# Kernel optimization log

Hardware: AMD Instinct MI355X
Metric: run time of the kernel (lower is better)

The kernel has to match this reference:

```python
import jax, jax.numpy as jnp
import numpy as np
from jax import lax

EPS = 1e-8  # numerical safety in squash sqrt (torch repo uses plain sqrt)

def squash(s, axis=-1):
    sq = jnp.sum(s * s, axis=axis, keepdims=True)
    return (sq / (1.0 + sq)) * s / jnp.sqrt(sq + EPS)

def conv2d(x, w, b, stride):
    y = lax.conv_general_dilated(x, w, (stride, stride), 'VALID',
                                 dimension_numbers=('NCHW', 'OIHW', 'NCHW'))
    return y + b[None, :, None, None]

def setup_inputs() -> dict:
    key = jax.random.key(0)
    ks = jax.random.split(key, 12)
    B = 256
    x = jax.random.normal(ks[0], (B, 1, 28, 28), dtype=jnp.float32)
    conv_w = jax.random.normal(ks[1], (256, 1, 9, 9), dtype=jnp.float32) * 0.05
    conv_b = jnp.zeros((256,), dtype=jnp.float32)
    caps1_w = jax.random.normal(ks[2], (32, 8, 256, 9, 9), dtype=jnp.float32) * 0.01
    caps1_b = jnp.zeros((32, 8), dtype=jnp.float32)
    caps2_w = jax.random.normal(ks[3], (10, 1152, 8, 16), dtype=jnp.float32)  # torch.randn
    dec_w1 = jax.random.normal(ks[4], (160, 512), dtype=jnp.float32) * 0.05
    dec_b1 = jnp.zeros((512,), dtype=jnp.float32)
    dec_w2 = jax.random.normal(ks[5], (512, 1024), dtype=jnp.float32) * 0.04
    dec_b2 = jnp.zeros((1024,), dtype=jnp.float32)
    dec_w3 = jax.random.normal(ks[6], (1024, 784), dtype=jnp.float32) * 0.03
    dec_b3 = jnp.zeros((784,), dtype=jnp.float32)
    return {"x": x, "conv_w": conv_w, "conv_b": conv_b, "caps1_w": caps1_w,
            "caps1_b": caps1_b, "caps2_w": caps2_w, "dec_w1": dec_w1,
            "dec_b1": dec_b1, "dec_w2": dec_w2, "dec_b2": dec_b2,
            "dec_w3": dec_w3, "dec_b3": dec_b3}

def reference(x, conv_w, conv_b, caps1_w, caps1_b, caps2_w,
              dec_w1, dec_b1, dec_w2, dec_b2, dec_w3, dec_b3):
    B = x.shape[0]
    # conv + relu -> [B,256,20,20]
    h = jax.nn.relu(conv2d(x, conv_w, conv_b, 1))
    # CapsLayerOne: 32 parallel convs folded into one grouped-out conv -> [B,256,6,6]
    u = conv2d(h, caps1_w.reshape(32 * 8, 256, 9, 9), caps1_b.reshape(-1), 2)
    u = u.reshape(B, 32, 8, 6, 6)                    # [B,caps,ch,h,w]
    # replicate torch cat(dim=-1).view(B,8,-1): flatten order (h, caps, w) per channel
    u = u.transpose(0, 2, 3, 1, 4).reshape(B, 8, 1152)  # [B,8,N]
    u = squash(u.transpose(0, 2, 1))                 # [B,N,8], N=1152
    # CapsLayerTwo dynamic routing
    x_hat = jnp.einsum('bni,cnio->cbno', u, caps2_w)[:, :, :, None, :]  # [10,B,N,1,16]
    b = jnp.zeros_like(x_hat)
    v = None
    for i in range(3):
        c = jax.nn.softmax(b, axis=2)
        s = jnp.sum(x_hat * c, axis=2, keepdims=True)  # [10,B,1,1,16]
        v = squash(s)
        if i != 2:
            b = b + jnp.sum(x_hat * v, axis=-1, keepdims=True)
    v = v[:, :, 0, 0, :].transpose(1, 0, 2)            # [B,10,16]
    class_scores = jnp.sqrt(jnp.sum(v * v, axis=-1) + EPS)  # [B,10]
    class_probabilities = jax.nn.softmax(class_scores, axis=-1)
    labels = jnp.argmax(class_probabilities, axis=1)
    y = jax.nn.one_hot(labels, 10, dtype=v.dtype)
    masked = (v * y[:, :, None]).reshape(B, 160)
    d = jax.nn.relu(masked @ dec_w1 + dec_b1)
    d = jax.nn.relu(d @ dec_w2 + dec_b2)
    reconstructions = jax.nn.sigmoid(d @ dec_w3 + dec_b3)  # [B,784]
    return (class_probabilities, reconstructions)
```

## Files before the change

kernel.cpp:

```cpp
#include <hip/hip_runtime.h>
#include <cstdint>
#include <cstddef>

#define EPSF 1e-8f

typedef __attribute__((ext_vector_type(8))) short bf16x8;
typedef __attribute__((ext_vector_type(4))) float f32x4;
typedef unsigned short ushort_t;

static __device__ __forceinline__ ushort_t f2bf(float f) {
  unsigned u = __builtin_bit_cast(unsigned, f);
  unsigned r = (u + 0x7FFFu + ((u >> 16) & 1u)) >> 16;
  return (ushort_t)r;
}
static __device__ __forceinline__ float bf2f(ushort_t h) {
  return __builtin_bit_cast(float, (unsigned)h << 16);
}

__global__ __launch_bounds__(256) void conv1_kernel(
    const float* __restrict__ x, const float* __restrict__ cw,
    const float* __restrict__ cb, ushort_t* __restrict__ h2hi, ushort_t* __restrict__ h2lo)
{
  int oy = blockIdx.x, b = blockIdx.y, ci = threadIdx.x;
  float w[81];
#pragma unroll
  for (int i = 0; i < 81; ++i) w[i] = cw[ci * 81 + i];
  float bias = cb[ci];
  float acc[20];
#pragma unroll
  for (int ox = 0; ox < 20; ++ox) acc[ox] = bias;
  const float* xb = x + (size_t)b * 784;
  for (int ky = 0; ky < 9; ++ky) {
    const float* row = xb + (oy + ky) * 28;
    float rv[28];
#pragma unroll
    for (int c = 0; c < 28; ++c) rv[c] = row[c];
#pragma unroll
    for (int kx = 0; kx < 9; ++kx) {
      float wv = w[ky * 9 + kx];
#pragma unroll
      for (int ox = 0; ox < 20; ++ox)
        acc[ox] = fmaf(rv[ox + kx], wv, acc[ox]);
    }
  }
#pragma unroll
  for (int ox = 0; ox < 20; ++ox) {
    float a = fmaxf(acc[ox], 0.f);
    ushort_t hi = f2bf(a);
    ushort_t lo = f2bf(a - bf2f(hi));
    size_t o = ((size_t)(b * 400 + oy * 20 + ox)) * 256 + ci;
    h2hi[o] = hi; h2lo[o] = lo;
  }
}

__global__ __launch_bounds__(256) void w2k_prep_kernel(
    const float* __restrict__ c1w, ushort_t* __restrict__ w2khi, ushort_t* __restrict__ w2klo)
{
  int co = blockIdx.x, ci = threadIdx.x;
  const float* src = c1w + ((size_t)co * 256 + ci) * 81;
  size_t dst = (size_t)co * 20736 + ci;
  for (int tap = 0; tap < 81; ++tap) {
    float v = src[tap];
    ushort_t hi = f2bf(v);
    w2khi[dst + (size_t)tap * 256] = hi;
    w2klo[dst + (size_t)tap * 256] = f2bf(v - bf2f(hi));
  }
}

__global__ __launch_bounds__(512, 1) void caps1_mfma_kernel(
    const ushort_t* __restrict__ h2hi, const ushort_t* __restrict__ h2lo,
    const ushort_t* __restrict__ w2khi, const ushort_t* __restrict__ w2klo,
    float* __restrict__ partial)
{
  int bid = blockIdx.x;
  int ks8  = bid & 7;
  int ks   = ks8 >> 1;
  int ktap = ks8 & 1;
  int rest = bid >> 3;
  int mt = rest & 1;
  int nt = (rest >> 1) & 1;
  int pos = rest >> 2;
  int ys = pos / 6, xs = pos % 6;
  int t = threadIdx.x;
  int wid = t >> 6, lane = t & 63;
  int wrow = wid >> 2, wcol = wid & 3;
  int lrow = lane & 15, g = lane >> 4;

  int b0 = mt * 128, n0 = nt * 128, cib = ks * 64;
  int tb    = ktap ? 41 : 0;
  int ntaps = ktap ? 40 : 41;

  __shared__ ushort_t lds[2][4][128 * 64];

  f32x4 acc[4][2];
#pragma unroll
  for (int i = 0; i < 4; ++i)
#pragma unroll
    for (int j = 0; j < 2; ++j) acc[i][j] = (f32x4){0.f, 0.f, 0.f, 0.f};

  int c_ = (t & 7) ^ ((t >> 3) & 7);
  size_t aRow[2], bRow[2];
  int ldsBase[2];
#pragma unroll
  for (int i = 0; i < 2; ++i) {
    int row = i * 64 + (t >> 3);
    aRow[i] = (size_t)(b0 + row) * 400 * 256 + cib + c_ * 8;
    bRow[i] = (size_t)(n0 + row) * 20736 + cib + c_ * 8;
    ldsBase[i] = (i * 64 + wid * 8) * 64;
  }

  auto stage = [&](int tap, int bufi) {
    int ky = tap / 9, kx = tap - ky * 9;
    int pix = (2 * ys + ky) * 20 + 2 * xs + kx;
    size_t aoff = (size_t)pix * 256;
    size_t boff = (size_t)tap * 256;
#pragma unroll
    for (int i = 0; i < 2; ++i) {
      __builtin_amdgcn_global_load_lds(h2hi + aRow[i] + aoff, &lds[bufi][0][ldsBase[i]], 16, 0, 0);
      __builtin_amdgcn_global_load_lds(h2lo + aRow[i] + aoff, &lds[bufi][1][ldsBase[i]], 16, 0, 0);
      __builtin_amdgcn_global_load_lds(w2khi + bRow[i] + boff, &lds[bufi][2][ldsBase[i]], 16, 0, 0);
      __builtin_amdgcn_global_load_lds(w2klo + bRow[i] + boff, &lds[bufi][3][ldsBase[i]], 16, 0, 0);
    }
  };

  stage(tb + 0, 0);
  stage(tb + 1, 1);
  asm volatile("s_waitcnt vmcnt(8)" ::: "memory");
  __builtin_amdgcn_sched_barrier(0);
  __builtin_amdgcn_s_barrier();

  for (int j = 0; j < ntaps; ++j) {
    int cur = j & 1;
    const ushort_t* LAh = &lds[cur][0][0];
    const ushort_t* LAl = &lds[cur][1][0];
    const ushort_t* LBh = &lds[cur][2][0];
    const ushort_t* LBl = &lds[cur][3][0];
    bf16x8 a_h[2][4], a_l[2][4], b_h[2][2], b_l[2][2];
#pragma unroll
    for (int kseg = 0; kseg < 2; ++kseg) {
#pragma unroll
      for (int mf = 0; mf < 4; ++mf) {
        int off = (wrow * 64 + mf * 16 + lrow) * 64 + ((kseg * 4 + g) ^ (lrow & 7)) * 8;
        a_h[kseg][mf] = *(const bf16x8*)(LAh + off);
        a_l[kseg][mf] = *(const bf16x8*)(LAl + off);
      }
#pragma unroll
      for (int nf = 0; nf < 2; ++nf) {
        int off = (wcol * 32 + nf * 16 + lrow) * 64 + ((kseg * 4 + g) ^ (lrow & 7)) * 8;
        b_h[kseg][nf] = *(const bf16x8*)(LBh + off);
        b_l[kseg][nf] = *(const bf16x8*)(LBl + off);
      }
    }
    asm volatile("s_waitcnt lgkmcnt(0)" ::: "memory");
    __builtin_amdgcn_sched_barrier(0);
    __builtin_amdgcn_s_barrier();

    if (j + 2 < ntaps) stage(tb + j + 2, cur);
    __builtin_amdgcn_sched_barrier(0);

    __builtin_amdgcn_s_setprio(1);
#pragma unroll
    for (int kseg = 0; kseg < 2; ++kseg)
#pragma unroll
      for (int mf = 0; mf < 4; ++mf)
#pragma unroll
        for (int nf = 0; nf < 2; ++nf) {
          acc[mf][nf] = __builtin_amdgcn_mfma_f32_16x16x32_bf16(a_h[kseg][mf], b_h[kseg][nf], acc[mf][nf], 0, 0, 0);
          acc[mf][nf] = __builtin_amdgcn_mfma_f32_16x16x32_bf16(a_h[kseg][mf], b_l[kseg][nf], acc[mf][nf], 0, 0, 0);
          acc[mf][nf] = __builtin_amdgcn_mfma_f32_16x16x32_bf16(a_l[kseg][mf], b_h[kseg][nf], acc[mf][nf], 0, 0, 0);
        }
    __builtin_amdgcn_s_setprio(0);
    __builtin_amdgcn_sched_barrier(0);

    if (j + 2 < ntaps) { asm volatile("s_waitcnt vmcnt(8)" ::: "memory"); }
    else               { asm volatile("s_waitcnt vmcnt(0)" ::: "memory"); }
    __builtin_amdgcn_sched_barrier(0);
    __builtin_amdgcn_s_barrier();
  }

  float* pp = partial + (size_t)ks8 * 2359296;
#pragma unroll
  for (int mf = 0; mf < 4; ++mf) {
    int m = b0 + wrow * 64 + mf * 16 + g * 4;
#pragma unroll
    for (int nf = 0; nf < 2; ++nf) {
      int n = n0 + wcol * 32 + nf * 16 + lrow;
#pragma unroll
      for (int r = 0; r < 4; ++r)
        pp[((size_t)(pos * 256 + m + r)) * 256 + n] = acc[mf][nf][r];
    }
  }
}

__global__ __launch_bounds__(256) void combine_kernel(
    const float* __restrict__ partial, const float* __restrict__ c1b, float* __restrict__ u)
{
  int gidx = blockIdx.x * 256 + threadIdx.x;
  int caps = gidx & 31;
  int b = (gidx >> 5) & 255;
  int pos = gidx >> 13;
  int ys = pos / 6, xs = pos % 6;
  size_t base = ((size_t)pos * 256 + b) * 256 + caps * 8;
  f32x4 s0 = {0.f, 0.f, 0.f, 0.f}, s1 = {0.f, 0.f, 0.f, 0.f};
#pragma unroll
  for (int ksp = 0; ksp < 8; ++ksp) {
    const float* pp = partial + (size_t)ksp * 2359296 + base;
    s0 += *(const f32x4*)pp;
    s1 += *(const f32x4*)(pp + 4);
  }
  const float* bp = c1b + caps * 8;
#pragma unroll
  for (int i = 0; i < 4; ++i) { s0[i] += bp[i]; s1[i] += bp[4 + i]; }
  float sq = s0[0]*s0[0] + s0[1]*s0[1] + s0[2]*s0[2] + s0[3]*s0[3]
           + s1[0]*s1[0] + s1[1]*s1[1] + s1[2]*s1[2] + s1[3]*s1[3];
  float scale = sq / ((1.f + sq) * sqrtf(sq + EPSF));
  int nvec = ys * 192 + caps * 6 + xs;
  float* up = u + ((size_t)b * 1152 + nvec) * 8;
  f32x4 o0, o1;
#pragma unroll
  for (int i = 0; i < 4; ++i) { o0[i] = s0[i] * scale; o1[i] = s1[i] * scale; }
  *(f32x4*)up = o0;
  *(f32x4*)(up + 4) = o1;
}

__global__ __launch_bounds__(320) void xhat_kernel(
    const float* __restrict__ u, const float* __restrict__ W2, float* __restrict__ xh)
{
  int np = blockIdx.x;
  int t = threadIdx.x;
  int nh = t / 160;
  int r  = t % 160;
  int c = r >> 4, o = r & 15;
  int n = np * 2 + nh;
  __shared__ float us[2][256][8];
  for (int e = t; e < 4096; e += 320) {
    int b = e >> 4;
    int nn = (e >> 3) & 1, i = e & 7;
    us[nn][b][i] = u[((size_t)b * 1152 + np * 2 + nn) * 8 + i];
  }
  __syncthreads();
  float wcol[8];
  const float* wp = W2 + (((size_t)c * 1152 + n) * 8) * 16 + o;
#pragma unroll
  for (int i = 0; i < 8; ++i) wcol[i] = wp[i * 16];
  float* xp = xh + ((size_t)(c * 256) * 1152 + n) * 16 + o;
  for (int b = 0; b < 256; ++b) {
    float s = 0.f;
#pragma unroll
    for (int i = 0; i < 8; ++i) s = fmaf(us[nh][b][i], wcol[i], s);
    xp[(size_t)b * 1152 * 16] = s;
  }
}

__global__ __launch_bounds__(256) void routing_kernel(
    const float* __restrict__ xhat, float* __restrict__ vout)
{
  int b = blockIdx.x, c = blockIdx.y, t = threadIdx.x;
  int wid = t >> 6, lane = t & 63;
  float xh[5][16];
  float bn[5] = {0, 0, 0, 0, 0};
  bool valid[5];
  const float* xp = xhat + ((size_t)(c * 256 + b)) * 1152 * 16;
#pragma unroll
  for (int j = 0; j < 5; ++j) {
    int n = t + 256 * j;
    valid[j] = (n < 1152);
    if (valid[j]) {
      const f32x4* q = (const f32x4*)(xp + (size_t)n * 16);
#pragma unroll
      for (int v4 = 0; v4 < 4; ++v4) {
        f32x4 val = q[v4];
#pragma unroll
        for (int k = 0; k < 4; ++k) xh[j][v4 * 4 + k] = val[k];
      }
    } else {
#pragma unroll
      for (int o = 0; o < 16; ++o) xh[j][o] = 0.f;
    }
  }
  __shared__ float redm[4], redz[4], reds[64], sv[16];
  float scale = 0.f;
  for (int it = 0; it < 3; ++it) {
    float m = -1e30f;
#pragma unroll
    for (int j = 0; j < 5; ++j) if (valid[j]) m = fmaxf(m, bn[j]);
    for (int d = 1; d < 64; d <<= 1) m = fmaxf(m, __shfl_xor(m, d));
    if (lane == 0) redm[wid] = m;
    __syncthreads();
    m = fmaxf(fmaxf(redm[0], redm[1]), fmaxf(redm[2], redm[3]));
    float e[5]; float z = 0.f;
#pragma unroll
    for (int j = 0; j < 5; ++j) { e[j] = valid[j] ? expf(bn[j] - m) : 0.f; z += e[j]; }
    for (int d = 1; d < 64; d <<= 1) z += __shfl_xor(z, d);
    if (lane == 0) redz[wid] = z;
    __syncthreads();
    z = redz[0] + redz[1] + redz[2] + redz[3];
    float ps[16];
#pragma unroll
    for (int o = 0; o < 16; ++o) ps[o] = 0.f;
#pragma unroll
    for (int j = 0; j < 5; ++j)
#pragma unroll
      for (int o = 0; o < 16; ++o) ps[o] = fmaf(e[j], xh[j][o], ps[o]);
#pragma unroll
    for (int o = 0; o < 16; ++o) {
      float vv = ps[o];
      for (int d = 1; d < 64; d <<= 1) vv += __shfl_xor(vv, d);
      if (lane == 0) reds[wid * 16 + o] = vv;
    }
    __syncthreads();
    if (t < 16) sv[t] = (reds[t] + reds[16 + t] + reds[32 + t] + reds[48 + t]) / z;
    __syncthreads();
    float vsc[16]; float sq = 0.f;
#pragma unroll
    for (int o = 0; o < 16; ++o) { vsc[o] = sv[o]; sq += sv[o] * sv[o]; }
    scale = sq / ((1.f + sq) * sqrtf(sq + EPSF));
    if (it < 2) {
#pragma unroll
      for (int j = 0; j < 5; ++j) if (valid[j]) {
        float dot = 0.f;
#pragma unroll
        for (int o = 0; o < 16; ++o) dot = fmaf(xh[j][o], vsc[o] * scale, dot);
        bn[j] += dot;
      }
    }
    __syncthreads();
  }
  if (t < 16) vout[((size_t)c * 256 + b) * 16 + t] = sv[t] * scale;
}

__global__ __launch_bounds__(256) void classify_kernel(
    const float* __restrict__ v, float* __restrict__ probs, float* __restrict__ masked)
{
  int b = blockIdx.x, t = threadIdx.x;
  __shared__ float sc[10], vv[160];
  int c = t >> 4, o = t & 15;
  float val = 0.f;
  if (t < 160) { val = v[((size_t)c * 256 + b) * 16 + o]; vv[t] = val; }
  float sq = val * val;
  sq += __shfl_xor(sq, 1); sq += __shfl_xor(sq, 2);
  sq += __shfl_xor(sq, 4); sq += __shfl_xor(sq, 8);
  if (t < 160 && o == 0) sc[c] = sqrtf(sq + EPSF);
  __syncthreads();
  float m = sc[0];
#pragma unroll
  for (int i = 1; i < 10; ++i) m = fmaxf(m, sc[i]);
  float ee[10]; float Z = 0.f;
#pragma unroll
  for (int i = 0; i < 10; ++i) { ee[i] = expf(sc[i] - m); Z += ee[i]; }
  float p[10];
#pragma unroll
  for (int i = 0; i < 10; ++i) p[i] = ee[i] / Z;
  int label = 0; float best = p[0];
#pragma unroll
  for (int i = 1; i < 10; ++i) if (p[i] > best) { best = p[i]; label = i; }
  if (t < 10) probs[(size_t)b * 10 + t] = p[t];
  if (t < 160) masked[(size_t)b * 160 + t] = (c == label) ? vv[t] : 0.f;
}

template <int ACT>
__global__ __launch_bounds__(256) void mlp_kernel(
    const float* __restrict__ A, const float* __restrict__ W,
    const float* __restrict__ bias, float* __restrict__ C, int N, int K)
{
  int j = blockIdx.x * 64 + (threadIdx.x & 63);
  int ty = threadIdx.x >> 6;
  int m0 = blockIdx.y * 16;
  __shared__ float As[16][33];
  float acc[4] = {0.f, 0.f, 0.f, 0.f};
  for (int k0 = 0; k0 < K; k0 += 32) {
    for (int e = threadIdx.x; e < 512; e += 256) {
      int r = e >> 5, kk = e & 31;
      As[r][kk] = A[(size_t)(m0 + r) * K + k0 + kk];
    }
    __syncthreads();
    if (j < N) {
      for (int kk = 0; kk < 32; ++kk) {
        float wv = W[(size_t)(k0 + kk) * N + j];
#pragma unroll
        for (int r = 0; r < 4; ++r) acc[r] = fmaf(As[ty + 4 * r][kk], wv, acc[r]);
      }
    }
    __syncthreads();
  }
  if (j < N) {
    float bv = bias[j];
#pragma unroll
    for (int r = 0; r < 4; ++r) {
      float xx = acc[r] + bv;
      if (ACT == 0) xx = fmaxf(xx, 0.f);
      else xx = 1.f / (1.f + expf(-xx));
      C[(size_t)(m0 + ty + 4 * r) * N + j] = xx;
    }
  }
}

extern "C" void kernel_launch(void* const* d_in, const int* in_sizes, int n_in,
                              void* d_out, int out_size, void* d_ws, size_t ws_size,
                              hipStream_t stream)
{
  const float* x   = (const float*)d_in[0];
  const float* cw  = (const float*)d_in[1];
  const float* cb  = (const float*)d_in[2];
  const float* c1w = (const float*)d_in[3];
  const float* c1b = (const float*)d_in[4];
  const float* c2w = (const float*)d_in[5];
  const float* w1  = (const float*)d_in[6];
  const float* b1  = (const float*)d_in[7];
  const float* w2  = (const float*)d_in[8];
  const float* b2  = (const float*)d_in[9];
  const float* w3  = (const float*)d_in[10];
  const float* b3  = (const float*)d_in[11];
  float* out = (float*)d_out;

  char* p = (char*)d_ws;
  float* xh = (float*)p;
  ushort_t* h2hi  = (ushort_t*)p; p += (size_t)26214400 * 2;
  ushort_t* h2lo  = (ushort_t*)p; p += (size_t)26214400 * 2;
  ushort_t* w2khi = (ushort_t*)p; p += (size_t)5308416 * 2;
  ushort_t* w2klo = (ushort_t*)p; p += (size_t)5308416 * 2;
  float* partial  = (float*)p;    p += (size_t)8 * 2359296 * 4;
  float* u        = (float*)p;    p += (size_t)2359296 * 4;
  float* v        = (float*)p;    p += (size_t)40960 * 4;
  float* masked   = (float*)p;    p += (size_t)40960 * 4;
  float* a1       = (float*)p;    p += (size_t)131072 * 4;
  float* a2       = (float*)p;    p += (size_t)262144 * 4;

  hipLaunchKernelGGL(w2k_prep_kernel, dim3(256), dim3(256), 0, stream, c1w, w2khi, w2klo);
  hipLaunchKernelGGL(conv1_kernel, dim3(20, 256), dim3(256), 0, stream, x, cw, cb, h2hi, h2lo);
  hipLaunchKernelGGL(caps1_mfma_kernel, dim3(1152), dim3(512), 0, stream, h2hi, h2lo, w2khi, w2klo, partial);
  hipLaunchKernelGGL(combine_kernel, dim3(1152), dim3(256), 0, stream, partial, c1b, u);
  hipLaunchKernelGGL(xhat_kernel, dim3(576), dim3(320), 0, stream, u, c2w, xh);
  hipLaunchKernelGGL(routing_kernel, dim3(256, 10), dim3(256), 0, stream, xh, v);
  hipLaunchKernelGGL(classify_kernel, dim3(256), dim3(256), 0, stream, v, out, masked);
  hipLaunchKernelGGL(mlp_kernel<0>, dim3(8, 16), dim3(256), 0, stream, masked, w1, b1, a1, 512, 160);
  hipLaunchKernelGGL(mlp_kernel<0>, dim3(16, 16), dim3(256), 0, stream, a1, w2, b2, a2, 1024, 512);
  hipLaunchKernelGGL(mlp_kernel<1>, dim3(13, 16), dim3(256), 0, stream, a2, w3, b3, out + 2560, 784, 1024);
}
```

Before: 623.5 us.

## Use 4 waves with 64x64 warp tiles and overlap LDS fragment reads with MFMA

The caps1 MFMA kernel drops from 8 to 4 waves per block, and each wave now computes a 64x64 tile with a 4x4 accumulator array. Each thread therefore issues twice as many global-to-LDS loads. The main loop is restructured so the next tile's global stage is issued first. Fragments for the next buffer are then read from LDS between the two k-segment MFMA batches, so LDS reads overlap with MFMA work. This raises register pressure and halves the waves available to hide latency, in exchange for more MFMA work per LDS read and software-pipelined fragment loads.

```diff
diff --git a/kernel.cpp b/kernel.cpp
--- a/kernel.cpp
+++ b/kernel.cpp
@@ -67,7 +67,7 @@
   }
 }
 
-__global__ __launch_bounds__(512, 1) void caps1_mfma_kernel(
+__global__ __launch_bounds__(256, 1) void caps1_mfma_kernel(
     const ushort_t* __restrict__ h2hi, const ushort_t* __restrict__ h2lo,
     const ushort_t* __restrict__ w2khi, const ushort_t* __restrict__ w2klo,
     float* __restrict__ partial)
@@ -83,7 +83,7 @@
   int ys = pos / 6, xs = pos % 6;
   int t = threadIdx.x;
   int wid = t >> 6, lane = t & 63;
-  int wrow = wid >> 2, wcol = wid & 3;
+  int wr = wid >> 1, wc = wid & 1;
   int lrow = lane & 15, g = lane >> 4;
 
   int b0 = mt * 128, n0 = nt * 128, cib = ks * 64;
@@ -92,99 +92,108 @@
 
   __shared__ ushort_t lds[2][4][128 * 64];
 
-  f32x4 acc[4][2];
+  f32x4 acc[4][4];
 #pragma unroll
   for (int i = 0; i < 4; ++i)
 #pragma unroll
-    for (int j = 0; j < 2; ++j) acc[i][j] = (f32x4){0.f, 0.f, 0.f, 0.f};
+    for (int j = 0; j < 4; ++j) acc[i][j] = (f32x4){0.f, 0.f, 0.f, 0.f};
 
   int c_ = (t & 7) ^ ((t >> 3) & 7);
-  size_t aRow[2], bRow[2];
-  int ldsBase[2];
-#pragma unroll
-  for (int i = 0; i < 2; ++i) {
-    int row = i * 64 + (t >> 3);
-    aRow[i] = (size_t)(b0 + row) * 400 * 256 + cib + c_ * 8;
-    bRow[i] = (size_t)(n0 + row) * 20736 + cib + c_ * 8;
-    ldsBase[i] = (i * 64 + wid * 8) * 64;
+  size_t aRow400[4], bRowC[4];
+  int ldsBase[4];
+#pragma unroll
+  for (int i = 0; i < 4; ++i) {
+    int row = i * 32 + (t >> 3);
+    aRow400[i] = (size_t)(b0 + row) * 400;
+    bRowC[i]   = (size_t)(n0 + row) * 20736 + cib + c_ * 8;
+    ldsBase[i] = (i * 32 + wid * 8) * 64;
   }
 
   auto stage = [&](int tap, int bufi) {
     int ky = tap / 9, kx = tap - ky * 9;
     int pix = (2 * ys + ky) * 20 + 2 * xs + kx;
-    size_t aoff = (size_t)pix * 256;
-    size_t boff = (size_t)tap * 256;
-#pragma unroll
-    for (int i = 0; i < 2; ++i) {
-      __builtin_amdgcn_global_load_lds(h2hi + aRow[i] + aoff, &lds[bufi][0][ldsBase[i]], 16, 0, 0);
-      __builtin_amdgcn_global_load_lds(h2lo + aRow[i] + aoff, &lds[bufi][1][ldsBase[i]], 16, 0, 0);
-      __builtin_amdgcn_global_load_lds(w2khi + bRow[i] + boff, &lds[bufi][2][ldsBase[i]], 16, 0, 0);
-      __builtin_amdgcn_global_load_lds(w2klo + bRow[i] + boff, &lds[bufi][3][ldsBase[i]], 16, 0, 0);
-    }
+#pragma unroll
+    for (int i = 0; i < 4; ++i) {
+      size_t ao = (aRow400[i] + pix) * 256 + cib + c_ * 8;
+      size_t bo = bRowC[i] + (size_t)tap * 256;
+      __builtin_amdgcn_global_load_lds(h2hi + ao, &lds[bufi][0][ldsBase[i]], 16, 0, 0);
+      __builtin_amdgcn_global_load_lds(h2lo + ao, &lds[bufi][1][ldsBase[i]], 16, 0, 0);
+      __builtin_amdgcn_global_load_lds(w2khi + bo, &lds[bufi][2][ldsBase[i]], 16, 0, 0);
+      __builtin_amdgcn_global_load_lds(w2klo + bo, &lds[bufi][3][ldsBase[i]], 16, 0, 0);
+    }
+  };
+
+  bf16x8 a_h[2][4], a_l[2][4], b_h[2][4], b_l[2][4];
+
+  auto read_frags_k = [&](int kseg, int bufi) {
+    const ushort_t* L0 = &lds[bufi][0][0];
+    const ushort_t* L1 = &lds[bufi][1][0];
+    const ushort_t* L2 = &lds[bufi][2][0];
+    const ushort_t* L3 = &lds[bufi][3][0];
+#pragma unroll
+    for (int f = 0; f < 4; ++f) {
+      int ra = wr * 64 + f * 16 + lrow;
+      int oa = ra * 64 + ((kseg * 4 + g) ^ (ra & 7)) * 8;
+      a_h[kseg][f] = *(const bf16x8*)(L0 + oa);
+      a_l[kseg][f] = *(const bf16x8*)(L1 + oa);
+      int rb = wc * 64 + f * 16 + lrow;
+      int ob = rb * 64 + ((kseg * 4 + g) ^ (rb & 7)) * 8;
+      b_h[kseg][f] = *(const bf16x8*)(L2 + ob);
+      b_l[kseg][f] = *(const bf16x8*)(L3 + ob);
+    }
+  };
+
+  auto mfma_kseg = [&](int kseg) {
+    __builtin_amdgcn_s_setprio(1);
+#pragma unroll
+    for (int mf = 0; mf < 4; ++mf)
+#pragma unroll
+      for (int nf = 0; nf < 4; ++nf) {
+        acc[mf][nf] = __builtin_amdgcn_mfma_f32_16x16x32_bf16(a_h[kseg][mf], b_h[kseg][nf], acc[mf][nf], 0, 0, 0);
+        acc[mf][nf] = __builtin_amdgcn_mfma_f32_16x16x32_bf16(a_h[kseg][mf], b_l[kseg][nf], acc[mf][nf], 0, 0, 0);
+        acc[mf][nf] = __builtin_amdgcn_mfma_f32_16x16x32_bf16(a_l[kseg][mf], b_h[kseg][nf], acc[mf][nf], 0, 0, 0);
+      }
+    __builtin_amdgcn_s_setprio(0);
   };
 
   stage(tb + 0, 0);
   stage(tb + 1, 1);
-  asm volatile("s_waitcnt vmcnt(8)" ::: "memory");
+  asm volatile("s_waitcnt vmcnt(16)" ::: "memory");
+  __builtin_amdgcn_s_barrier();
+  asm volatile("" ::: "memory");
+  read_frags_k(0, 0);
+  read_frags_k(1, 0);
+  asm volatile("s_waitcnt lgkmcnt(0)" ::: "memory");
   __builtin_amdgcn_sched_barrier(0);
   __builtin_amdgcn_s_barrier();
+  asm volatile("" ::: "memory");
 
   for (int j = 0; j < ntaps; ++j) {
     int cur = j & 1;
-    const ushort_t* LAh = &lds[cur][0][0];
-    const ushort_t* LAl = &lds[cur][1][0];
-    const ushort_t* LBh = &lds[cur][2][0];
-    const ushort_t* LBl = &lds[cur][3][0];
-    bf16x8 a_h[2][4], a_l[2][4], b_h[2][2], b_l[2][2];
-#pragma unroll
-    for (int kseg = 0; kseg < 2; ++kseg) {
-#pragma unroll
-      for (int mf = 0; mf < 4; ++mf) {
-        int off = (wrow * 64 + mf * 16 + lrow) * 64 + ((kseg * 4 + g) ^ (lrow & 7)) * 8;
-        a_h[kseg][mf] = *(const bf16x8*)(LAh + off);
-        a_l[kseg][mf] = *(const bf16x8*)(LAl + off);
-      }
-#pragma unroll
-      for (int nf = 0; nf < 2; ++nf) {
-        int off = (wcol * 32 + nf * 16 + lrow) * 64 + ((kseg * 4 + g) ^ (lrow & 7)) * 8;
-        b_h[kseg][nf] = *(const bf16x8*)(LBh + off);
-        b_l[kseg][nf] = *(const bf16x8*)(LBl + off);
-      }
-    }
+    if (j + 2 < ntaps) stage(tb + j + 2, cur);
+    mfma_kseg(0);
+    if (j + 1 < ntaps) {
+      if (j + 2 < ntaps) { asm volatile("s_waitcnt vmcnt(16)" ::: "memory"); }
+      else               { asm volatile("s_waitcnt vmcnt(0)" ::: "memory"); }
+      __builtin_amdgcn_s_barrier();
+      asm volatile("" ::: "memory");
+      read_frags_k(0, cur ^ 1);
+    }
+    mfma_kseg(1);
+    if (j + 1 < ntaps) read_frags_k(1, cur ^ 1);
     asm volatile("s_waitcnt lgkmcnt(0)" ::: "memory");
     __builtin_amdgcn_sched_barrier(0);
     __builtin_amdgcn_s_barrier();
-
-    if (j + 2 < ntaps) stage(tb + j + 2, cur);
-    __builtin_amdgcn_sched_barrier(0);
-
-    __builtin_amdgcn_s_setprio(1);
-#pragma unroll
-    for (int kseg = 0; kseg < 2; ++kseg)
-#pragma unroll
-      for (int mf = 0; mf < 4; ++mf)
-#pragma unroll
-        for (int nf = 0; nf < 2; ++nf) {
-          acc[mf][nf] = __builtin_amdgcn_mfma_f32_16x16x32_bf16(a_h[kseg][mf], b_h[kseg][nf], acc[mf][nf], 0, 0, 0);
-          acc[mf][nf] = __builtin_amdgcn_mfma_f32_16x16x32_bf16(a_h[kseg][mf], b_l[kseg][nf], acc[mf][nf], 0, 0, 0);
-          acc[mf][nf] = __builtin_amdgcn_mfma_f32_16x16x32_bf16(a_l[kseg][mf], b_h[kseg][nf], acc[mf][nf], 0, 0, 0);
-        }
-    __builtin_amdgcn_s_setprio(0);
-    __builtin_amdgcn_sched_barrier(0);
-
-    if (j + 2 < ntaps) { asm volatile("s_waitcnt vmcnt(8)" ::: "memory"); }
-    else               { asm volatile("s_waitcnt vmcnt(0)" ::: "memory"); }
-    __builtin_amdgcn_sched_barrier(0);
-    __builtin_amdgcn_s_barrier();
+    asm volatile("" ::: "memory");
   }
 
   float* pp = partial + (size_t)ks8 * 2359296;
 #pragma unroll
   for (int mf = 0; mf < 4; ++mf) {
-    int m = b0 + wrow * 64 + mf * 16 + g * 4;
-#pragma unroll
-    for (int nf = 0; nf < 2; ++nf) {
-      int n = n0 + wcol * 32 + nf * 16 + lrow;
+    int m = b0 + wr * 64 + mf * 16 + g * 4;
+#pragma unroll
+    for (int nf = 0; nf < 4; ++nf) {
+      int n = n0 + wc * 64 + nf * 16 + lrow;
 #pragma unroll
       for (int r = 0; r < 4; ++r)
         pp[((size_t)(pos * 256 + m + r)) * 256 + n] = acc[mf][nf][r];
@@ -428,7 +437,7 @@
 
   hipLaunchKernelGGL(w2k_prep_kernel, dim3(256), dim3(256), 0, stream, c1w, w2khi, w2klo);
   hipLaunchKernelGGL(conv1_kernel, dim3(20, 256), dim3(256), 0, stream, x, cw, cb, h2hi, h2lo);
-  hipLaunchKernelGGL(caps1_mfma_kernel, dim3(1152), dim3(512), 0, stream, h2hi, h2lo, w2khi, w2klo, partial);
+  hipLaunchKernelGGL(caps1_mfma_kernel, dim3(1152), dim3(256), 0, stream, h2hi, h2lo, w2khi, w2klo, partial);
   hipLaunchKernelGGL(combine_kernel, dim3(1152), dim3(256), 0, stream, partial, c1b, u);
   hipLaunchKernelGGL(xhat_kernel, dim3(576), dim3(320), 0, stream, u, c2w, xh);
   hipLaunchKernelGGL(routing_kernel, dim3(256, 10), dim3(256), 0, stream, xh, v);
```

Result: slower. 664.4 us (+6.6%).
